# Kernel tuning notes

Hardware: AMD Instinct MI355X
Metric: run time of the kernel (lower is better)

Reference implementation:

```python
import jax, jax.numpy as jnp
import numpy as np

SPARSITY = 0.9

def setup_inputs() -> dict:
    key = jax.random.key(0)
    k1, k2, k3 = jax.random.split(key, 3)
    B, IN, OUT = 8192, 4096, 4096
    x = jax.random.normal(k1, (B, IN), dtype=jnp.float32)
    weight = jax.random.normal(k2, (OUT, IN), dtype=jnp.float32)
    mask = jax.random.uniform(k3, (OUT, IN)) > SPARSITY
    weight = weight * mask.astype(jnp.float32)  # pre-masked, like weight.to_sparse()
    bias = jnp.zeros((OUT,), dtype=jnp.float32)
    return {"x": x, "weight": weight, "bias": bias, "mask": mask}

def reference(x, weight, bias, mask):
    # out = (W_sparse @ x.T).T + b  ==  x @ W.T + b with W zero off-pattern
    w = weight * mask.astype(weight.dtype)
    out = jnp.einsum('bi,oi->bo', x, w) + bias  # [B, OUT]
    return out
```

## Files before the change

kernel.cpp:

```cpp
#include <hip/hip_runtime.h>
#include <hip/hip_bf16.h>

#define M_DIM 8192
#define N_DIM 4096
#define K_DIM 4096

using bf16x8 = __attribute__((ext_vector_type(8))) short;
using f32x4  = __attribute__((ext_vector_type(4))) float;

__device__ __forceinline__ unsigned short f2bf(float f) {
    unsigned int u = __float_as_uint(f);
    unsigned int r = u + 0x7fffu + ((u >> 16) & 1u);
    return (unsigned short)(r >> 16);
}

__global__ void cvt_both_f32_to_bf16(const float* __restrict__ x,
                                     const float* __restrict__ w,
                                     unsigned short* __restrict__ ws,
                                     int n4x, int n4w) {
    int i = blockIdx.x * blockDim.x + threadIdx.x;
    const int stride = gridDim.x * blockDim.x;
    const int total = n4x + n4w;
    uint2* dx = reinterpret_cast<uint2*>(ws);
    uint2* dw = reinterpret_cast<uint2*>(ws) + n4x;
    for (; i < total; i += stride) {
        const bool isX = i < n4x;
        const float4* s4 = isX ? reinterpret_cast<const float4*>(x)
                               : reinterpret_cast<const float4*>(w);
        const int j = isX ? i : i - n4x;
        float4 v = s4[j];
        uint2 o;
        o.x = (unsigned)f2bf(v.x) | ((unsigned)f2bf(v.y) << 16);
        o.y = (unsigned)f2bf(v.z) | ((unsigned)f2bf(v.w) << 16);
        (isX ? dx : dw)[j] = o;
    }
}

__device__ __forceinline__ void gload16(const unsigned short* g, char* l) {
    __builtin_amdgcn_global_load_lds(
        (const __attribute__((address_space(1))) void*)g,
        (__attribute__((address_space(3))) void*)l, 16, 0, 0);
}

__global__ __launch_bounds__(512, 2) void gemm_bf16_256_8ph(
        const unsigned short* __restrict__ xb,
        const unsigned short* __restrict__ wb,
        const float* __restrict__ bias,
        float* __restrict__ out) {
    extern __shared__ char lds[];
    char* ldsA = lds;
    char* ldsB = lds + 65536;

    const int bid = blockIdx.x;
    const int xcd = bid & 7;
    const int c   = bid >> 3;
    const int tm  = (xcd >> 1) * 8 + (c & 7);
    const int tn  = (xcd & 1) * 8 + (c >> 3);
    const int r0 = tm * 256;
    const int c0 = tn * 256;

    const int tid  = threadIdx.x;
    const int lane = tid & 63;
    const int wave = tid >> 6;
    const int wm = wave >> 2;
    const int wn = wave & 3;
    const int lr = lane & 15;
    const int t4 = lane >> 4;

    int aRd[4][2], bRd[2][2];
    const int swz = (lr & 7) << 4;
#pragma unroll
    for (int ks = 0; ks < 2; ++ks) {
        const int cb = (ks * 64 + t4 * 16) ^ swz;
#pragma unroll
        for (int m = 0; m < 4; ++m)
            aRd[m][ks] = (wm * 64 + m * 16 + lr) * 128 + cb;
#pragma unroll
        for (int n = 0; n < 2; ++n)
            bRd[n][ks] = (wn * 32 + n * 16 + lr) * 128 + cb;
    }

    const int rowInBlk = lane >> 3;
    const int sChunk   = ((lane & 7) ^ rowInBlk) * 8;
    int aSrcB[2], bSrcB[2], dstOff[2];
#pragma unroll
    for (int l = 0; l < 2; ++l) {
        const int R0 = wave * 16 + l * 8;
        aSrcB[l] = (r0 + (R0 >> 6) * 128 + (R0 & 63) + rowInBlk) * K_DIM + sChunk;
        bSrcB[l] = (c0 + (R0 >> 5) * 64  + (R0 & 31) + rowInBlk) * K_DIM + sChunk;
        dstOff[l] = R0 * 128;
    }

    auto STAGE_A = [&](int q, int kt, int nb) {
#pragma unroll
        for (int l = 0; l < 2; ++l)
            gload16(xb + aSrcB[l] + q * 64 * K_DIM + kt * 64,
                    ldsA + nb * 32768 + q * 16384 + dstOff[l]);
    };
    auto STAGE_B = [&](int p, int kt, int nb) {
#pragma unroll
        for (int l = 0; l < 2; ++l)
            gload16(wb + bSrcB[l] + p * 32 * K_DIM + kt * 64,
                    ldsB + nb * 32768 + p * 16384 + dstOff[l]);
    };

    f32x4 acc[8][4];
#pragma unroll
    for (int i = 0; i < 8; ++i)
#pragma unroll
        for (int j = 0; j < 4; ++j)
            acc[i][j] = (f32x4){0.f, 0.f, 0.f, 0.f};

    bf16x8 av[4][2], bv0[2][2], bv1[2][2];

#define MFMA_QUAD(M0, N0, BV)                                                  \
    do {                                                                       \
        __builtin_amdgcn_s_setprio(1);                                         \
        _Pragma("unroll") for (int m = 0; m < 4; ++m)                          \
        _Pragma("unroll") for (int n = 0; n < 2; ++n)                          \
        _Pragma("unroll") for (int ks = 0; ks < 2; ++ks)                       \
            acc[(M0) + m][(N0) + n] = __builtin_amdgcn_mfma_f32_16x16x32_bf16( \
                av[m][ks], BV[n][ks], acc[(M0) + m][(N0) + n], 0, 0, 0);       \
        __builtin_amdgcn_s_setprio(0);                                         \
    } while (0)

#define LOAD_A(Q, BUF)                                                         \
    _Pragma("unroll") for (int m = 0; m < 4; ++m)                              \
    _Pragma("unroll") for (int ks = 0; ks < 2; ++ks)                           \
        av[m][ks] = *(const bf16x8*)(ldsA + (BUF) * 32768 + (Q) * 16384 + aRd[m][ks]);

#define LOAD_B(P, BUF, BV)                                                     \
    _Pragma("unroll") for (int n = 0; n < 2; ++n)                              \
    _Pragma("unroll") for (int ks = 0; ks < 2; ++ks)                           \
        BV[n][ks] = *(const bf16x8*)(ldsB + (BUF) * 32768 + (P) * 16384 + bRd[n][ks]);

    STAGE_A(0, 0, 0);
    STAGE_B(0, 0, 0);
    STAGE_B(1, 0, 0);
    STAGE_A(1, 0, 0);
    STAGE_A(0, 1, 1);
    STAGE_B(0, 1, 1);
    STAGE_B(1, 1, 1);
    asm volatile("s_waitcnt vmcnt(6)\n\ts_barrier" ::: "memory");

    const int NT = K_DIM / 64;
    for (int t = 0; t < NT; ++t) {
        const int buf = t & 1, nbuf = buf ^ 1;
        const int kt1 = (t + 1) & (NT - 1);
        const int kt2 = (t + 2) & (NT - 1);
        LOAD_A(0, buf);
        LOAD_B(0, buf, bv0);
        STAGE_A(1, kt1, nbuf);
        MFMA_QUAD(0, 0, bv0);
        asm volatile("s_barrier" ::: "memory");
        LOAD_B(1, buf, bv1);
        STAGE_A(0, kt2, buf);
        MFMA_QUAD(0, 2, bv1);
        asm volatile("s_barrier" ::: "memory");
        LOAD_A(1, buf);
        STAGE_B(0, kt2, buf);
        MFMA_QUAD(4, 2, bv1);
        asm volatile("s_barrier" ::: "memory");
        STAGE_B(1, kt2, buf);
        MFMA_QUAD(4, 0, bv0);
        asm volatile("s_waitcnt vmcnt(6)\n\ts_barrier" ::: "memory");
    }
    asm volatile("s_waitcnt vmcnt(0)" ::: "memory");

#pragma unroll
    for (int ni = 0; ni < 4; ++ni) {
        const int col = c0 + wn * 64 + (ni >> 1) * 32 + (ni & 1) * 16 + lr;
        const float bvs = bias[col];
#pragma unroll
        for (int mi = 0; mi < 8; ++mi) {
            const int row0 = r0 + wm * 128 + (mi >> 2) * 64 + (mi & 3) * 16 + t4 * 4;
#pragma unroll
            for (int j = 0; j < 4; ++j)
                out[(row0 + j) * N_DIM + col] = acc[mi][ni][j] + bvs;
        }
    }
#undef MFMA_QUAD
#undef LOAD_A
#undef LOAD_B
}

__global__ __launch_bounds__(256) void gemm_bf16_mfma(
        const unsigned short* __restrict__ xb,
        const unsigned short* __restrict__ wb,
        const float* __restrict__ bias,
        float* __restrict__ out) {
    __shared__ unsigned short sA[128 * 64];
    __shared__ unsigned short sB[128 * 64];

    const int nwg = (M_DIM / 128) * (N_DIM / 128);
    const int q = nwg / 8;
    int bid = blockIdx.x;
    int bid2 = (bid & 7) * q + (bid >> 3);
    const int tm = bid2 & 63;
    const int tn = bid2 >> 6;
    const int r0 = tm * 128;
    const int c0 = tn * 128;

    const int tid  = threadIdx.x;
    const int lane = tid & 63;
    const int wave = tid >> 6;
    const int wr = wave >> 1;
    const int wc = wave & 1;
    const int lr = lane & 15;
    const int t  = lane >> 4;

    int aoff[2][4], boff[2][4];
#pragma unroll
    for (int m = 0; m < 4; ++m) {
        int rowA = wr * 64 + m * 16 + lr;
        int swA  = (rowA & 7) << 4;
        int rowB = wc * 64 + m * 16 + lr;
        int swB  = (rowB & 7) << 4;
#pragma unroll
        for (int kk = 0; kk < 2; ++kk) {
            int cb = kk * 64 + t * 16;
            aoff[kk][m] = rowA * 64 + ((cb ^ swA) >> 1);
            boff[kk][m] = rowB * 64 + ((cb ^ swB) >> 1);
        }
    }

    const int sRow   = lane >> 3;
    const int sChunk = (lane & 7) ^ sRow;
    int aSrc[4], bSrc[4];
    char* ldsA[4];
    char* ldsB[4];
#pragma unroll
    for (int r = 0; r < 4; ++r) {
        int row = r * 32 + wave * 8 + sRow;
        aSrc[r] = (r0 + row) * K_DIM + sChunk * 8;
        bSrc[r] = (c0 + row) * K_DIM + sChunk * 8;
        ldsA[r] = (char*)sA + (r * 4 + wave) * 1024;
        ldsB[r] = (char*)sB + (r * 4 + wave) * 1024;
    }

    f32x4 acc[4][4];
#pragma unroll
    for (int m = 0; m < 4; ++m)
#pragma unroll
        for (int n = 0; n < 4; ++n)
            acc[m][n] = (f32x4){0.f, 0.f, 0.f, 0.f};

    for (int kt = 0; kt < K_DIM / 64; ++kt) {
        const int ko = kt * 64;
#pragma unroll
        for (int r = 0; r < 4; ++r) {
            gload16(xb + aSrc[r] + ko, ldsA[r]);
            gload16(wb + bSrc[r] + ko, ldsB[r]);
        }
        __syncthreads();
#pragma unroll
        for (int kk = 0; kk < 2; ++kk) {
            bf16x8 av[4], bv[4];
#pragma unroll
            for (int m = 0; m < 4; ++m)
                av[m] = *reinterpret_cast<const bf16x8*>(sA + aoff[kk][m]);
#pragma unroll
            for (int n = 0; n < 4; ++n)
                bv[n] = *reinterpret_cast<const bf16x8*>(sB + boff[kk][n]);
#pragma unroll
            for (int m = 0; m < 4; ++m)
#pragma unroll
                for (int n = 0; n < 4; ++n)
                    acc[m][n] = __builtin_amdgcn_mfma_f32_16x16x32_bf16(
                        av[m], bv[n], acc[m][n], 0, 0, 0);
        }
        __syncthreads();
    }

#pragma unroll
    for (int n = 0; n < 4; ++n) {
        const int col = c0 + wc * 64 + n * 16 + lr;
        const float bv = bias[col];
#pragma unroll
        for (int m = 0; m < 4; ++m) {
            const int row0 = r0 + wr * 64 + m * 16 + t * 4;
#pragma unroll
            for (int j = 0; j < 4; ++j)
                out[(row0 + j) * N_DIM + col] = acc[m][n][j] + bv;
        }
    }
}

__global__ void fallback_gemm_f32(const float* __restrict__ x,
                                  const float* __restrict__ w,
                                  const float* __restrict__ bias,
                                  float* __restrict__ out) {
    __shared__ float sX[2][4096];
    const int tid = threadIdx.x;
    const int col = blockIdx.x * 256 + tid;
    const int row0 = blockIdx.y * 2;
    for (int i = tid * 4; i < 8192; i += 1024) {
        int r = i >> 12, c = i & 4095;
        *(float4*)&sX[r][c] = *(const float4*)&x[(size_t)(row0 + r) * 4096 + c];
    }
    __syncthreads();
    const float4* wrow = (const float4*)&w[(size_t)col * 4096];
    float a0 = 0.f, a1 = 0.f;
    for (int k4 = 0; k4 < 1024; ++k4) {
        float4 wv = wrow[k4];
        int k = k4 << 2;
        a0 += wv.x * sX[0][k] + wv.y * sX[0][k + 1] + wv.z * sX[0][k + 2] + wv.w * sX[0][k + 3];
        a1 += wv.x * sX[1][k] + wv.y * sX[1][k + 1] + wv.z * sX[1][k + 2] + wv.w * sX[1][k + 3];
    }
    float bv = bias[col];
    out[(size_t)row0 * 4096 + col] = a0 + bv;
    out[(size_t)(row0 + 1) * 4096 + col] = a1 + bv;
}

extern "C" void kernel_launch(void* const* d_in, const int* in_sizes, int n_in,
                              void* d_out, int out_size, void* d_ws, size_t ws_size,
                              hipStream_t stream) {
    const float* x    = (const float*)d_in[0];
    const float* w    = (const float*)d_in[1];
    const float* bias = (const float*)d_in[2];
    float* out = (float*)d_out;

    const size_t nX = (size_t)M_DIM * K_DIM;
    const size_t nW = (size_t)N_DIM * K_DIM;
    const size_t need = (nX + nW) * sizeof(unsigned short);

    if (ws_size >= need) {
        unsigned short* xb = (unsigned short*)d_ws;
        unsigned short* wb = xb + nX;
        cvt_both_f32_to_bf16<<<3072, 256, 0, stream>>>(
            x, w, (unsigned short*)d_ws, (int)(nX / 4), (int)(nW / 4));
        hipError_t e = hipFuncSetAttribute(
            (const void*)gemm_bf16_256_8ph,
            hipFuncAttributeMaxDynamicSharedMemorySize, 131072);
        if (e == hipSuccess) {
            gemm_bf16_256_8ph<<<(M_DIM / 256) * (N_DIM / 256), 512, 131072, stream>>>(
                xb, wb, bias, out);
        } else {
            gemm_bf16_mfma<<<(M_DIM / 128) * (N_DIM / 128), 256, 0, stream>>>(
                xb, wb, bias, out);
        }
    } else {
        fallback_gemm_f32<<<dim3(N_DIM / 256, M_DIM / 2), 256, 0, stream>>>(x, w, bias, out);
    }
}
```

Baseline: 264.3 us.

## Prefetch next tile's LDS fragments with ping-pong registers across unrolled K loop

Restructures the main K loop so the next tile's A0/B0 fragments are read from shared memory into registers during the current tile's last phases. Two B register sets alternate, with the loop unrolled by two. The schedule of global staging, LDS reads and vmcnt waits inside each tile is reordered so LDS latency overlaps the MFMA work. This is meant to hide LDS read stalls at tile boundaries. The cost is extra register pressure and a more delicate hazard ordering between buffers.

```diff
diff --git a/kernel.cpp b/kernel.cpp
--- a/kernel.cpp
+++ b/kernel.cpp
@@ -111,7 +111,7 @@
         for (int j = 0; j < 4; ++j)
             acc[i][j] = (f32x4){0.f, 0.f, 0.f, 0.f};
 
-    bf16x8 av[4][2], bv0[2][2], bv1[2][2];
+    bf16x8 av[4][2], bvA[2][2], bvB[2][2], bv1[2][2];
 
 #define MFMA_QUAD(M0, N0, BV)                                                  \
     do {                                                                       \
@@ -134,6 +134,35 @@
     _Pragma("unroll") for (int ks = 0; ks < 2; ++ks)                           \
         BV[n][ks] = *(const bf16x8*)(ldsB + (BUF) * 32768 + (P) * 16384 + bRd[n][ks]);
 
+    const int NT = K_DIM / 64;
+
+#define TILE_BODY(T, BUF, XV, YV)                                              \
+    do {                                                                       \
+        const int nb_  = (BUF) ^ 1;                                           \
+        const int kt1_ = ((T) + 1) & (NT - 1);                                 \
+        const int kt2_ = ((T) + 2) & (NT - 1);                                 \
+                                      \
+        STAGE_A(1, kt1_, nb_);                                                 \
+        LOAD_B(1, (BUF), bv1);                                                 \
+        MFMA_QUAD(0, 0, XV);                                                   \
+        asm volatile("s_barrier" ::: "memory");                                \
+                   \
+        STAGE_A(0, kt2_, (BUF));                                               \
+        MFMA_QUAD(0, 2, bv1);                                                  \
+        LOAD_A(1, (BUF));                                                      \
+        asm volatile("s_waitcnt vmcnt(6)\n\ts_barrier" ::: "memory");          \
+                               \
+        STAGE_B(0, kt2_, (BUF));                                               \
+        LOAD_B(0, nb_, YV);                                                    \
+        MFMA_QUAD(4, 2, bv1);                                                  \
+        asm volatile("s_barrier" ::: "memory");                                \
+                   \
+        STAGE_B(1, kt2_, (BUF));                                               \
+        MFMA_QUAD(4, 0, XV);                                                   \
+        LOAD_A(0, nb_);                                                        \
+        asm volatile("s_waitcnt vmcnt(6)\n\ts_barrier" ::: "memory");          \
+    } while (0)
+
     STAGE_A(0, 0, 0);
     STAGE_B(0, 0, 0);
     STAGE_B(1, 0, 0);
@@ -142,28 +171,12 @@
     STAGE_B(0, 1, 1);
     STAGE_B(1, 1, 1);
     asm volatile("s_waitcnt vmcnt(6)\n\ts_barrier" ::: "memory");
-
-    const int NT = K_DIM / 64;
-    for (int t = 0; t < NT; ++t) {
-        const int buf = t & 1, nbuf = buf ^ 1;
-        const int kt1 = (t + 1) & (NT - 1);
-        const int kt2 = (t + 2) & (NT - 1);
-        LOAD_A(0, buf);
-        LOAD_B(0, buf, bv0);
-        STAGE_A(1, kt1, nbuf);
-        MFMA_QUAD(0, 0, bv0);
-        asm volatile("s_barrier" ::: "memory");
-        LOAD_B(1, buf, bv1);
-        STAGE_A(0, kt2, buf);
-        MFMA_QUAD(0, 2, bv1);
-        asm volatile("s_barrier" ::: "memory");
-        LOAD_A(1, buf);
-        STAGE_B(0, kt2, buf);
-        MFMA_QUAD(4, 2, bv1);
-        asm volatile("s_barrier" ::: "memory");
-        STAGE_B(1, kt2, buf);
-        MFMA_QUAD(4, 0, bv0);
-        asm volatile("s_waitcnt vmcnt(6)\n\ts_barrier" ::: "memory");
+    LOAD_A(0, 0);
+    LOAD_B(0, 0, bvA);
+
+    for (int tt = 0; tt < NT / 2; ++tt) {
+        TILE_BODY(2 * tt,     0, bvA, bvB);
+        TILE_BODY(2 * tt + 1, 1, bvB, bvA);
     }
     asm volatile("s_waitcnt vmcnt(0)" ::: "memory");
 
@@ -179,6 +192,7 @@
                 out[(row0 + j) * N_DIM + col] = acc[mi][ni][j] + bvs;
         }
     }
+#undef TILE_BODY
 #undef MFMA_QUAD
 #undef LOAD_A
 #undef LOAD_B
```

Measured after the change: 260.8 us. No clear change (-1.3%).
